# Kernel optimization log

Hardware: AMD Instinct MI355X
Metric: run time of the kernel (lower is better)

The kernel has to match this reference:

```python
import jax, jax.numpy as jnp
import numpy as np

B, T, H, Z = 128, 1024, 256, 64


def setup_inputs() -> dict:
    key = jax.random.key(0)
    k1, k2, k3, k4 = jax.random.split(key, 4)
    scale = 1.0 / np.sqrt(H + Z)
    return {
        "input_q": jax.random.normal(k1, (B, T, H), dtype=jnp.float32),
        "eps": jax.random.normal(k2, (B, T, Z), dtype=jnp.float32),
        "W_mu": jax.random.normal(k3, (Z, H + Z), dtype=jnp.float32) * scale,
        "b_mu": jnp.zeros((Z,), dtype=jnp.float32),
        "W_std": jax.random.normal(k4, (Z, H + Z), dtype=jnp.float32) * scale,
        "b_std": jnp.zeros((Z,), dtype=jnp.float32),
    }


def reference(input_q, eps, W_mu, b_mu, W_std, b_std):
    # Recurrent sampling: z_t = mu(h_t, z_{t-1}) + eps_t * std(h_t, z_{t-1})
    h_seq = jnp.swapaxes(input_q, 0, 1)  # [T, B, H]
    e_seq = jnp.swapaxes(eps, 0, 1)      # [T, B, Z]

    def step(z_prev, inp):
        h_t, e_t = inp
        x = jnp.concatenate([h_t, z_prev], axis=-1)          # [B, H+Z]
        mu = x @ W_mu.T + b_mu                               # [B, Z]
        std = jax.nn.softplus(x @ W_std.T + b_std) + 1e-4    # [B, Z]
        z = mu + e_t * std
        return z, (z, mu, std)

    z0 = jnp.zeros((B, Z), dtype=input_q.dtype)
    _, (z_seq, mu_seq, std_seq) = jax.lax.scan(step, z0, (h_seq, e_seq))
    # stack outputs back to [B, T, Z]
    z_seq = jnp.swapaxes(z_seq, 0, 1)
    mu_seq = jnp.swapaxes(mu_seq, 0, 1)
    std_seq = jnp.swapaxes(std_seq, 0, 1)
    return (z_seq, mu_seq, std_seq)
```

## Files before the change

### kernel.cpp

```cpp
#include <hip/hip_runtime.h>
#include <math.h>

#define B_ 128
#define T_ 1024
#define H_ 256
#define Z_ 64
#define M_ (B_ * T_)

typedef _Float16 h2 __attribute__((ext_vector_type(2)));
typedef _Float16 h4 __attribute__((ext_vector_type(4)));

__global__ __launch_bounds__(256) void precompute_kernel(
    const float* __restrict__ Hm,
    const float* __restrict__ Wmu,
    const float* __restrict__ Wstd,
    const float* __restrict__ bmu,
    const float* __restrict__ bstd,
    float* __restrict__ pre_mu,
    float* __restrict__ pre_std)
{
    const int tid = threadIdx.x;
    const int ty = tid >> 4;
    const int tx = tid & 15;
    const int m0 = blockIdx.x * 64;

    __shared__ float Ash[64][17];
    __shared__ float Wm[64][17];
    __shared__ float Ws[64][17];

    float accm[4][4] = {};
    float accs[4][4] = {};

    const int lrow = tid >> 2;
    const int lk   = (tid & 3) * 4;

    for (int k0 = 0; k0 < 256; k0 += 16) {
        float4 av  = *reinterpret_cast<const float4*>(&Hm[(size_t)(m0 + lrow) * H_ + k0 + lk]);
        float4 wmv = *reinterpret_cast<const float4*>(&Wmu[(size_t)lrow * 320 + k0 + lk]);
        float4 wsv = *reinterpret_cast<const float4*>(&Wstd[(size_t)lrow * 320 + k0 + lk]);
        __syncthreads();
        Ash[lrow][lk + 0] = av.x;  Ash[lrow][lk + 1] = av.y;
        Ash[lrow][lk + 2] = av.z;  Ash[lrow][lk + 3] = av.w;
        Wm[lrow][lk + 0] = wmv.x;  Wm[lrow][lk + 1] = wmv.y;
        Wm[lrow][lk + 2] = wmv.z;  Wm[lrow][lk + 3] = wmv.w;
        Ws[lrow][lk + 0] = wsv.x;  Ws[lrow][lk + 1] = wsv.y;
        Ws[lrow][lk + 2] = wsv.z;  Ws[lrow][lk + 3] = wsv.w;
        __syncthreads();

        #pragma unroll
        for (int kk = 0; kk < 16; ++kk) {
            float a4[4], wm4[4], ws4[4];
            #pragma unroll
            for (int i = 0; i < 4; ++i) a4[i] = Ash[ty * 4 + i][kk];
            #pragma unroll
            for (int jj = 0; jj < 4; ++jj) wm4[jj] = Wm[tx * 4 + jj][kk];
            #pragma unroll
            for (int jj = 0; jj < 4; ++jj) ws4[jj] = Ws[tx * 4 + jj][kk];
            #pragma unroll
            for (int i = 0; i < 4; ++i)
                #pragma unroll
                for (int jj = 0; jj < 4; ++jj) {
                    accm[i][jj] += a4[i] * wm4[jj];
                    accs[i][jj] += a4[i] * ws4[jj];
                }
        }
    }

    float4 bm = *reinterpret_cast<const float4*>(&bmu[tx * 4]);
    float4 bs = *reinterpret_cast<const float4*>(&bstd[tx * 4]);
    #pragma unroll
    for (int i = 0; i < 4; ++i) {
        const size_t m = (size_t)(m0 + ty * 4 + i);
        float4 om, os;
        om.x = accm[i][0] + bm.x;  om.y = accm[i][1] + bm.y;
        om.z = accm[i][2] + bm.z;  om.w = accm[i][3] + bm.w;
        os.x = accs[i][0] + bs.x;  os.y = accs[i][1] + bs.y;
        os.z = accs[i][2] + bs.z;  os.w = accs[i][3] + bs.w;
        *reinterpret_cast<float4*>(&pre_mu[m * Z_ + tx * 4])  = om;
        *reinterpret_cast<float4*>(&pre_std[m * Z_ + tx * 4]) = os;
    }
}

__global__ __launch_bounds__(64)
__attribute__((amdgpu_waves_per_eu(1, 1)))
void recurrent_kernel(
    const float* __restrict__ pre_mu,
    const float* __restrict__ pre_std,
    const float* __restrict__ eps,
    const float* __restrict__ Wmu,
    const float* __restrict__ Wstd,
    float* __restrict__ out)
{
    const int b = blockIdx.x;
    const int j = threadIdx.x;

    h2 wmuh[32], wstdh[32];
    {
        const float4* wm4 = reinterpret_cast<const float4*>(&Wmu[(size_t)j * 320 + 256]);
        const float4* ws4 = reinterpret_cast<const float4*>(&Wstd[(size_t)j * 320 + 256]);
        #pragma unroll
        for (int k = 0; k < 16; ++k) {
            const float4 a = wm4[k];
            const float4 s = ws4[k];
            wmuh[2 * k + 0] = (h2){(_Float16)a.x, (_Float16)a.y};
            wmuh[2 * k + 1] = (h2){(_Float16)a.z, (_Float16)a.w};
            wstdh[2 * k + 0] = (h2){(_Float16)s.x, (_Float16)s.y};
            wstdh[2 * k + 1] = (h2){(_Float16)s.z, (_Float16)s.w};
        }
        #pragma unroll
        for (int k = 0; k < 32; ++k) {
            asm volatile("" : "+v"(wmuh[k]));
            asm volatile("" : "+v"(wstdh[k]));
        }
    }

    __shared__ __align__(16) _Float16 zs[2][64];

    const size_t base = (size_t)b * T_ * Z_;
    float* __restrict__ zo   = out;
    float* __restrict__ muo  = out + (size_t)M_ * Z_;
    float* __restrict__ stdo = out + (size_t)2 * M_ * Z_;

    float pm0 = pre_mu[base + j];
    float ps0 = pre_std[base + j];
    float ev0 = eps[base + j];
    float pm1 = pre_mu[base + Z_ + j];
    float ps1 = pre_std[base + Z_ + j];
    float ev1 = eps[base + Z_ + j];

    float z = 0.0f;

    for (int t = 0; t < T_; ++t) {
        _Float16* zrow = zs[t & 1];
        zrow[j] = (_Float16)z;
        asm volatile("s_waitcnt lgkmcnt(0)" ::: "memory");

        float pm2 = 0.f, ps2 = 0.f, ev2 = 0.f;
        if (t + 2 < T_) {
            const size_t idx = base + (size_t)(t + 2) * Z_ + j;
            pm2 = pre_mu[idx];
            ps2 = pre_std[idx];
            ev2 = eps[idx];
        }

        const h4* __restrict__ z4 = reinterpret_cast<const h4*>(zrow);
        float am[4] = {pm0, 0.f, 0.f, 0.f};
        float as[4] = {ps0, 0.f, 0.f, 0.f};
        #pragma unroll
        for (int k = 0; k < 16; ++k) {
            const h4 q = z4[k];
            const h2 lo = __builtin_shufflevector(q, q, 0, 1);
            const h2 hi = __builtin_shufflevector(q, q, 2, 3);
            const int a = k & 3;
            am[a] = __builtin_amdgcn_fdot2(lo, wmuh[2 * k + 0], am[a], false);
            as[a] = __builtin_amdgcn_fdot2(lo, wstdh[2 * k + 0], as[a], false);
            am[a] = __builtin_amdgcn_fdot2(hi, wmuh[2 * k + 1], am[a], false);
            as[a] = __builtin_amdgcn_fdot2(hi, wstdh[2 * k + 1], as[a], false);
        }
        const float mu = (am[0] + am[1]) + (am[2] + am[3]);
        const float sx = (as[0] + as[1]) + (as[2] + as[3]);
        const float sp = (sx > 20.0f) ? sx : __logf(1.0f + __expf(sx));
        const float sd = sp + 1e-4f;
        z = mu + ev0 * sd;

        const size_t o = base + (size_t)t * Z_ + j;
        zo[o]   = z;
        muo[o]  = mu;
        stdo[o] = sd;

        pm0 = pm1; ps0 = ps1; ev0 = ev1;
        pm1 = pm2; ps1 = ps2; ev1 = ev2;
    }
}

extern "C" void kernel_launch(void* const* d_in, const int* in_sizes, int n_in,
                              void* d_out, int out_size, void* d_ws, size_t ws_size,
                              hipStream_t stream) {
    const float* input_q = (const float*)d_in[0];
    const float* eps     = (const float*)d_in[1];
    const float* W_mu    = (const float*)d_in[2];
    const float* b_mu    = (const float*)d_in[3];
    const float* W_std   = (const float*)d_in[4];
    const float* b_std   = (const float*)d_in[5];
    float* out = (float*)d_out;

    float* pre_mu  = (float*)d_ws;
    float* pre_std = pre_mu + (size_t)M_ * Z_;

    precompute_kernel<<<M_ / 64, 256, 0, stream>>>(
        input_q, W_mu, W_std, b_mu, b_std, pre_mu, pre_std);

    recurrent_kernel<<<B_, 64, 0, stream>>>(
        pre_mu, pre_std, eps, W_mu, W_std, out);
}
```

Measured before the change: 605.4 us.

## Process two independent batch sequences per wavefront to interleave recurrent dependency chains

Each recurrent block now handles two batch rows (b and b+64), interleaving their dot-product chains so the two independent recurrences hide each other's LDS and ALU latency. The grid is halved to 64 blocks, leaving fewer CUs busy, and register use roughly doubles for the prefetched inputs. The z write to shared memory moves to the end of the step, after the compute, for the next iteration.

After: 935.0 us. 1.54x slower.

```diff
diff --git a/kernel.cpp b/kernel.cpp
--- a/kernel.cpp
+++ b/kernel.cpp
@@ -114,62 +114,81 @@
         }
     }
 
-    __shared__ __align__(16) _Float16 zs[2][64];
-
-    const size_t base = (size_t)b * T_ * Z_;
+    __shared__ __align__(16) _Float16 zsA[2][64];
+    __shared__ __align__(16) _Float16 zsB[2][64];
+
+    const size_t baseA = (size_t)b * T_ * Z_;
+    const size_t baseB = (size_t)(b + 64) * T_ * Z_;
     float* __restrict__ zo   = out;
     float* __restrict__ muo  = out + (size_t)M_ * Z_;
     float* __restrict__ stdo = out + (size_t)2 * M_ * Z_;
 
-    float pm0 = pre_mu[base + j];
-    float ps0 = pre_std[base + j];
-    float ev0 = eps[base + j];
-    float pm1 = pre_mu[base + Z_ + j];
-    float ps1 = pre_std[base + Z_ + j];
-    float ev1 = eps[base + Z_ + j];
-
-    float z = 0.0f;
+    float pmA0 = pre_mu[baseA + j], psA0 = pre_std[baseA + j], evA0 = eps[baseA + j];
+    float pmB0 = pre_mu[baseB + j], psB0 = pre_std[baseB + j], evB0 = eps[baseB + j];
+    float pmA1 = pre_mu[baseA + Z_ + j], psA1 = pre_std[baseA + Z_ + j], evA1 = eps[baseA + Z_ + j];
+    float pmB1 = pre_mu[baseB + Z_ + j], psB1 = pre_std[baseB + Z_ + j], evB1 = eps[baseB + Z_ + j];
+
+    zsA[0][j] = (_Float16)0.0f;
+    zsB[0][j] = (_Float16)0.0f;
 
     for (int t = 0; t < T_; ++t) {
-        _Float16* zrow = zs[t & 1];
-        zrow[j] = (_Float16)z;
         asm volatile("s_waitcnt lgkmcnt(0)" ::: "memory");
 
-        float pm2 = 0.f, ps2 = 0.f, ev2 = 0.f;
+        float pmA2 = 0.f, psA2 = 0.f, evA2 = 0.f;
+        float pmB2 = 0.f, psB2 = 0.f, evB2 = 0.f;
         if (t + 2 < T_) {
-            const size_t idx = base + (size_t)(t + 2) * Z_ + j;
-            pm2 = pre_mu[idx];
-            ps2 = pre_std[idx];
-            ev2 = eps[idx];
-        }
-
-        const h4* __restrict__ z4 = reinterpret_cast<const h4*>(zrow);
-        float am[4] = {pm0, 0.f, 0.f, 0.f};
-        float as[4] = {ps0, 0.f, 0.f, 0.f};
+            const size_t ia = baseA + (size_t)(t + 2) * Z_ + j;
+            const size_t ib = baseB + (size_t)(t + 2) * Z_ + j;
+            pmA2 = pre_mu[ia];  psA2 = pre_std[ia];  evA2 = eps[ia];
+            pmB2 = pre_mu[ib];  psB2 = pre_std[ib];  evB2 = eps[ib];
+        }
+
+        const h4* __restrict__ z4A = reinterpret_cast<const h4*>(zsA[t & 1]);
+        const h4* __restrict__ z4B = reinterpret_cast<const h4*>(zsB[t & 1]);
+        float amA[4] = {pmA0, 0.f, 0.f, 0.f}, asA[4] = {psA0, 0.f, 0.f, 0.f};
+        float amB[4] = {pmB0, 0.f, 0.f, 0.f}, asB[4] = {psB0, 0.f, 0.f, 0.f};
         #pragma unroll
         for (int k = 0; k < 16; ++k) {
-            const h4 q = z4[k];
-            const h2 lo = __builtin_shufflevector(q, q, 0, 1);
-            const h2 hi = __builtin_shufflevector(q, q, 2, 3);
+            const h4 qA = z4A[k];
+            const h4 qB = z4B[k];
+            const h2 loA = __builtin_shufflevector(qA, qA, 0, 1);
+            const h2 hiA = __builtin_shufflevector(qA, qA, 2, 3);
+            const h2 loB = __builtin_shufflevector(qB, qB, 0, 1);
+            const h2 hiB = __builtin_shufflevector(qB, qB, 2, 3);
             const int a = k & 3;
-            am[a] = __builtin_amdgcn_fdot2(lo, wmuh[2 * k + 0], am[a], false);
-            as[a] = __builtin_amdgcn_fdot2(lo, wstdh[2 * k + 0], as[a], false);
-            am[a] = __builtin_amdgcn_fdot2(hi, wmuh[2 * k + 1], am[a], false);
-            as[a] = __builtin_amdgcn_fdot2(hi, wstdh[2 * k + 1], as[a], false);
-        }
-        const float mu = (am[0] + am[1]) + (am[2] + am[3]);
-        const float sx = (as[0] + as[1]) + (as[2] + as[3]);
-        const float sp = (sx > 20.0f) ? sx : __logf(1.0f + __expf(sx));
-        const float sd = sp + 1e-4f;
-        z = mu + ev0 * sd;
-
-        const size_t o = base + (size_t)t * Z_ + j;
-        zo[o]   = z;
-        muo[o]  = mu;
-        stdo[o] = sd;
-
-        pm0 = pm1; ps0 = ps1; ev0 = ev1;
-        pm1 = pm2; ps1 = ps2; ev1 = ev2;
+            amA[a] = __builtin_amdgcn_fdot2(loA, wmuh[2 * k + 0], amA[a], false);
+            amB[a] = __builtin_amdgcn_fdot2(loB, wmuh[2 * k + 0], amB[a], false);
+            asA[a] = __builtin_amdgcn_fdot2(loA, wstdh[2 * k + 0], asA[a], false);
+            asB[a] = __builtin_amdgcn_fdot2(loB, wstdh[2 * k + 0], asB[a], false);
+            amA[a] = __builtin_amdgcn_fdot2(hiA, wmuh[2 * k + 1], amA[a], false);
+            amB[a] = __builtin_amdgcn_fdot2(hiB, wmuh[2 * k + 1], amB[a], false);
+            asA[a] = __builtin_amdgcn_fdot2(hiA, wstdh[2 * k + 1], asA[a], false);
+            asB[a] = __builtin_amdgcn_fdot2(hiB, wstdh[2 * k + 1], asB[a], false);
+        }
+        const float muA = (amA[0] + amA[1]) + (amA[2] + amA[3]);
+        const float sxA = (asA[0] + asA[1]) + (asA[2] + asA[3]);
+        const float muB = (amB[0] + amB[1]) + (amB[2] + amB[3]);
+        const float sxB = (asB[0] + asB[1]) + (asB[2] + asB[3]);
+        const float spA = (sxA > 20.0f) ? sxA : __logf(1.0f + __expf(sxA));
+        const float spB = (sxB > 20.0f) ? sxB : __logf(1.0f + __expf(sxB));
+        const float sdA = spA + 1e-4f;
+        const float sdB = spB + 1e-4f;
+        const float zA = muA + evA0 * sdA;
+        const float zB = muB + evB0 * sdB;
+
+        zsA[(t + 1) & 1][j] = (_Float16)zA;
+        zsB[(t + 1) & 1][j] = (_Float16)zB;
+
+        const size_t oA = baseA + (size_t)t * Z_ + j;
+        const size_t oB = baseB + (size_t)t * Z_ + j;
+        zo[oA]   = zA;   zo[oB]   = zB;
+        muo[oA]  = muA;  muo[oB]  = muB;
+        stdo[oA] = sdA;  stdo[oB] = sdB;
+
+        pmA0 = pmA1; psA0 = psA1; evA0 = evA1;
+        pmB0 = pmB1; psB0 = psB1; evB0 = evB1;
+        pmA1 = pmA2; psA1 = psA2; evA1 = evA2;
+        pmB1 = pmB2; psB1 = psB2; evB1 = evB2;
     }
 }
 
@@ -190,6 +209,6 @@
     precompute_kernel<<<M_ / 64, 256, 0, stream>>>(
         input_q, W_mu, W_std, b_mu, b_std, pre_mu, pre_std);
 
-    recurrent_kernel<<<B_, 64, 0, stream>>>(
+    recurrent_kernel<<<B_ / 2, 64, 0, stream>>>(
         pre_mu, pre_std, eps, W_mu, W_std, out);
 }
```
